# Performance work log

Measured on AMD Instinct MI355X. Metric: run time of the kernel, lower is better.

The kernel has to match this reference:

```python
import jax, jax.numpy as jnp
import numpy as np

D_MODEL = 1024
N_HEADS = 16
HEAD_DIM = D_MODEL // N_HEADS


def setup_inputs() -> dict:
    key = jax.random.key(0)
    k_x, k_qkv, k_out = jax.random.split(key, 3)
    x = jax.random.normal(k_x, (4, 2048, D_MODEL), dtype=jnp.float32)
    # nn.Linear weights are (out_features, in_features); init std=0.02
    w_qkv = jax.random.normal(k_qkv, (3 * D_MODEL, D_MODEL), dtype=jnp.float32) * 0.02
    w_out = jax.random.normal(k_out, (D_MODEL, D_MODEL), dtype=jnp.float32) * 0.02
    return {"x": x, "w_qkv": w_qkv, "w_out": w_out}


def reference(x, w_qkv, w_out):
    B, T, C = x.shape
    H, Dh = N_HEADS, HEAD_DIM
    # qkv projection: x @ w_qkv.T -> (B, T, 3C)
    qkv = jnp.einsum('btc,oc->bto', x, w_qkv)
    q, k, v = jnp.split(qkv, 3, axis=-1)

    def split_heads(t):
        return t.reshape(B, T, H, Dh).transpose(0, 2, 1, 3)  # (B, H, T, Dh)

    q, k, v = split_heads(q), split_heads(k), split_heads(v)
    scale = jnp.sqrt(jnp.asarray(Dh, dtype=x.dtype))
    scores = jnp.einsum('bhqd,bhkd->bhqk', q, k) / scale  # (B, H, T, T)
    causal = jnp.tril(jnp.ones((T, T), dtype=bool))
    scores = jnp.where(causal[None, None], scores, jnp.asarray(-jnp.inf, dtype=scores.dtype))
    attn = jax.nn.softmax(scores, axis=-1)
    out = jnp.einsum('bhqk,bhkd->bhqd', attn, v)  # (B, H, T, Dh)
    out = out.transpose(0, 2, 1, 3).reshape(B, T, C)
    return jnp.einsum('btc,oc->bto', out, w_out)
```

## Files before the change

### kernel.cpp

```cpp
#include <hip/hip_runtime.h>

typedef __attribute__((ext_vector_type(8))) short bf16x8;
typedef __attribute__((ext_vector_type(4))) float f32x4;
typedef __attribute__((ext_vector_type(16))) float f32x16;
typedef __attribute__((ext_vector_type(4))) int i32x4;
using u16 = unsigned short;

constexpr int Bsz = 4, T = 2048, C = 1024, H = 16, Dh = 64;
constexpr int Mrows = Bsz * T;
constexpr int K_DIM = 1024;
constexpr float QSCALE = 0.18033688011112042f;

__device__ inline u16 f2bf(float f) {
    unsigned u = __builtin_bit_cast(unsigned, f);
    u += 0x7FFFu + ((u >> 16) & 1u);
    return (u16)(u >> 16);
}

__device__ inline void g2l16(const void* g, void* l) {
    __builtin_amdgcn_global_load_lds((const __attribute__((address_space(1))) void*)g,
                                     (__attribute__((address_space(3))) void*)l, 16, 0, 0);
}

__device__ inline unsigned pk2(float lo, float hi) {
    unsigned d;
    asm("v_cvt_pk_bf16_f32 %0, %1, %2" : "=v"(d) : "v"(lo), "v"(hi));
    return d;
}
__device__ inline void swap32(unsigned& a, unsigned& b) {
    asm("v_permlane32_swap_b32 %0, %1" : "+v"(a), "+v"(b));
}

__global__ __launch_bounds__(256)
void cvt_k(const float* __restrict__ x, const float* __restrict__ wq,
           const float* __restrict__ wo, u16* __restrict__ xb,
           u16* __restrict__ wqb, u16* __restrict__ wob)
{
    int idx = blockIdx.x * 256 + threadIdx.x;
    const float* src; u16* dst; int rel;
    if (idx < 1048576)      { src = x;  dst = xb;  rel = idx; }
    else if (idx < 1441792) { src = wq; dst = wqb; rel = idx - 1048576; }
    else                    { src = wo; dst = wob; rel = idx - 1441792; }
    size_t off = (size_t)rel * 8;
    float4 a = *(const float4*)(src + off);
    float4 b = *(const float4*)(src + off + 4);
    unsigned r0 = (unsigned)f2bf(a.x) | ((unsigned)f2bf(a.y) << 16);
    unsigned r1 = (unsigned)f2bf(a.z) | ((unsigned)f2bf(a.w) << 16);
    unsigned r2 = (unsigned)f2bf(b.x) | ((unsigned)f2bf(b.y) << 16);
    unsigned r3 = (unsigned)f2bf(b.z) | ((unsigned)f2bf(b.w) << 16);
    *(uint4*)(dst + off) = make_uint4(r0, r1, r2, r3);
}

__device__ inline void stage_g(u16* lds, const u16* gb, int ldg, int tid) {
    #pragma unroll
    for (int i = 0; i < 4; ++i) {
        int ch = i * 256 + tid;
        int r = ch >> 3, c8 = ch & 7;
        int sc = c8 ^ (r & 7);
        g2l16(gb + (size_t)r * ldg + sc * 8, lds + (i * 256 + (tid & 192)) * 8);
    }
}

template<int MODE>
__device__ __forceinline__
void gemm_body(const u16* __restrict__ Ab, const u16* __restrict__ Bb,
               float* __restrict__ Op, u16* __restrict__ qws,
               u16* __restrict__ kws, u16* __restrict__ vtws,
               u16* As, u16* Bs, int m0, int n0)
{
    const int tid = threadIdx.x;
    const int l = tid & 63, wid = tid >> 6;
    const int wm = wid >> 1, wn = wid & 1;
    const int lane16 = l & 15, lhi = l >> 4;

    const u16* Abase = Ab + (size_t)m0 * K_DIM;
    const u16* Bbase = Bb + (size_t)n0 * K_DIM;

    f32x4 acc[4][4] = {};

    for (int ks = 0; ks < K_DIM / 64; ++ks) {
        __syncthreads();
        stage_g(As, Abase + ks * 64, K_DIM, tid);
        stage_g(Bs, Bbase + ks * 64, K_DIM, tid);
        __syncthreads();
        #pragma unroll
        for (int kc = 0; kc < 2; kc++) {
            bf16x8 af[4], bfr[4];
            #pragma unroll
            for (int mi = 0; mi < 4; mi++) {
                int row = wm * 64 + mi * 16 + lane16;
                int byte = row * 128 + kc * 64 + lhi * 16; byte ^= (row & 7) << 4;
                af[mi] = *(const bf16x8*)((const char*)As + byte);
            }
            #pragma unroll
            for (int ni = 0; ni < 4; ni++) {
                int row = wn * 64 + ni * 16 + lane16;
                int byte = row * 128 + kc * 64 + lhi * 16; byte ^= (row & 7) << 4;
                bfr[ni] = *(const bf16x8*)((const char*)Bs + byte);
            }
            #pragma unroll
            for (int mi = 0; mi < 4; mi++)
                #pragma unroll
                for (int ni = 0; ni < 4; ni++) {
                    if constexpr (MODE == 2)
                        acc[mi][ni] = __builtin_amdgcn_mfma_f32_16x16x32_bf16(
                            bfr[ni], af[mi], acc[mi][ni], 0, 0, 0);
                    else
                        acc[mi][ni] = __builtin_amdgcn_mfma_f32_16x16x32_bf16(
                            af[mi], bfr[ni], acc[mi][ni], 0, 0, 0);
                }
        }
    }

    if constexpr (MODE == 2) {
        #pragma unroll
        for (int mi = 0; mi < 4; mi++)
            #pragma unroll
            for (int ni = 0; ni < 4; ni++)
                #pragma unroll
                for (int r = 0; r < 4; r++) {
                    int wr = n0 + wn * 64 + ni * 16 + lhi * 4 + r;
                    int tg = m0 + wm * 64 + mi * 16 + lane16;
                    int hh = (wr >> 6) & 15, d = wr & 63;
                    int bb = tg >> 11, tt = tg & 2047;
                    size_t off = (((size_t)bb * H + hh) * Dh + d) * T + tt;
                    vtws[off] = f2bf(acc[mi][ni][r]);
                }
    } else {
        #pragma unroll
        for (int mi = 0; mi < 4; mi++)
            #pragma unroll
            for (int ni = 0; ni < 4; ni++)
                #pragma unroll
                for (int r = 0; r < 4; r++) {
                    int gm = m0 + wm * 64 + mi * 16 + lhi * 4 + r;
                    int gn = n0 + wn * 64 + ni * 16 + lane16;
                    float val = acc[mi][ni][r];
                    if constexpr (MODE == 0) {
                        int hh = (gn >> 6) & 15, d = gn & 63;
                        int bb = gm >> 11, t = gm & 2047;
                        size_t off = (((size_t)bb * H + hh) * T + t) * Dh + d;
                        if (gn < C) qws[off] = f2bf(val * QSCALE);
                        else        kws[off] = f2bf(val);
                    } else {
                        Op[(size_t)gm * C + gn] = val;
                    }
                }
    }
}

__global__ __launch_bounds__(256)
void gemm_qkv(const u16* __restrict__ xb, const u16* __restrict__ wqkvb,
              u16* __restrict__ qws, u16* __restrict__ kws, u16* __restrict__ vtws)
{
    __shared__ alignas(16) u16 As[128 * 64];
    __shared__ alignas(16) u16 Bs[128 * 64];
    const int m0 = blockIdx.x * 128;
    if (blockIdx.y < 16)
        gemm_body<0>(xb, wqkvb, nullptr, qws, kws, vtws, As, Bs, m0, blockIdx.y * 128);
    else
        gemm_body<2>(xb, wqkvb, nullptr, qws, kws, vtws, As, Bs, m0,
                     2 * C + (blockIdx.y - 16) * 128);
}

__global__ __launch_bounds__(256)
void gemm_out(const u16* __restrict__ ob, const u16* __restrict__ woutb,
              float* __restrict__ Op)
{
    __shared__ alignas(16) u16 As[128 * 64];
    __shared__ alignas(16) u16 Bs[128 * 64];
    gemm_body<1>(ob, woutb, Op, nullptr, nullptr, nullptr, As, Bs,
                 blockIdx.x * 128, blockIdx.y * 128);
}

constexpr float SMAX = 16.0f;

__device__ inline void stage_c(u16* lds, const u16* gb, int rstride, int tid) {
    #pragma unroll
    for (int it = 0; it < 2; ++it) {
        int i = it * 256 + tid;
        int r = i & 63, c8 = i >> 6;
        g2l16(gb + (size_t)r * rstride + c8 * 8, lds + i * 8);
    }
}

__global__ __launch_bounds__(256, 3)
void attn_k(const u16* __restrict__ qws, const u16* __restrict__ kws,
            const u16* __restrict__ vtws, u16* __restrict__ ows)
{
    __shared__ alignas(16) u16 KL[3][64 * 64];
    __shared__ alignas(16) u16 VL[3][64 * 64];

    const int bid = blockIdx.x;
    const int head = bid & 63;
    const int qt = 15 - (bid >> 6);
    const int b = head >> 4, h = head & 15;
    const int tid = threadIdx.x, w = tid >> 6, l = tid & 63;
    const int l31 = l & 31, hi = l >> 5;

    const size_t hoff = (size_t)head * (T * Dh);
    const u16* Qg  = qws + hoff;
    const u16* Kg  = kws + hoff;
    const u16* Vtg = vtws + hoff;

    const int qb = qt * 128;
    const int nt = 2 * qt + 2;
    const int qbw = qb + w * 32;

    bf16x8 qf[4];
    #pragma unroll
    for (int c = 0; c < 4; ++c)
        qf[c] = *(const bf16x8*)(Qg + (size_t)(qbw + l31) * Dh + c * 16 + hi * 8);

    f32x16 o0{}, o1{};
    float lrun = 0.f;

    stage_c(KL[0], Kg, Dh, tid);
    stage_c(VL[0], Vtg, T, tid);
    stage_c(KL[1], Kg + (size_t)64 * Dh, Dh, tid);
    stage_c(VL[1], Vtg + 64, T, tid);

    int cur = 0;
    for (int t = 0; t < nt; ++t) {
        if (t + 1 < nt) asm volatile("s_waitcnt vmcnt(4)" ::: "memory");
        else            asm volatile("s_waitcnt vmcnt(0)" ::: "memory");
        __builtin_amdgcn_s_barrier();
        __builtin_amdgcn_sched_barrier(0);

        int nx = cur + 2; if (nx >= 3) nx -= 3;
        if (t + 2 < nt) {
            stage_c(KL[nx], Kg + (size_t)(t + 2) * 64 * Dh, Dh, tid);
            stage_c(VL[nx], Vtg + (t + 2) * 64, T, tid);
        }

        const int kv0 = t * 64;
        if (kv0 <= qbw + 31) {
            const char* Kb = (const char*)KL[cur];
            const char* Vb = (const char*)VL[cur];

            bf16x8 kf0[4], kf1[4];
            #pragma unroll
            for (int c = 0; c < 4; ++c) {
                int off = (c * 2 + hi) * 1024 + l31 * 16;
                kf0[c] = *(const bf16x8*)(Kb + off);
                kf1[c] = *(const bf16x8*)(Kb + off + 512);
            }

            f32x16 s0{}, s1{};
            __builtin_amdgcn_s_setprio(1);
            #pragma unroll
            for (int c = 0; c < 4; ++c) {
                s0 = __builtin_amdgcn_mfma_f32_32x32x16_bf16(kf0[c], qf[c], s0, 0, 0, 0);
                s1 = __builtin_amdgcn_mfma_f32_32x32x16_bf16(kf1[c], qf[c], s1, 0, 0, 0);
            }
            __builtin_amdgcn_s_setprio(0);

            if (kv0 + 63 > qbw) {
                int qg = qbw + l31;
                #pragma unroll
                for (int r = 0; r < 16; ++r) {
                    int kvg = kv0 + (r & 3) + 8 * (r >> 2) + 4 * hi;
                    if (kvg > qg)      s0[r] = -__builtin_inff();
                    if (kvg + 32 > qg) s1[r] = -__builtin_inff();
                }
            }

            float p0[16], p1[16];
            float t0 = 0.f, t1 = 0.f, t2 = 0.f, t3 = 0.f;
            #pragma unroll
            for (int r = 0; r < 16; ++r) {
                p0[r] = __builtin_amdgcn_exp2f(s0[r] - SMAX);
                p1[r] = __builtin_amdgcn_exp2f(s1[r] - SMAX);
                float s = p0[r] + p1[r];
                if ((r & 3) == 0) t0 += s; else if ((r & 3) == 1) t1 += s;
                else if ((r & 3) == 2) t2 += s; else t3 += s;
            }
            lrun += (t0 + t1) + (t2 + t3);

            unsigned paf[4][4];
            unsigned cc[8];
            #pragma unroll
            for (int i = 0; i < 4; ++i) cc[i]     = pk2(p0[2 * i], p0[2 * i + 1]);
            #pragma unroll
            for (int i = 0; i < 4; ++i) cc[4 + i] = pk2(p0[8 + 2 * i], p0[9 + 2 * i]);
            swap32(cc[0], cc[2]); swap32(cc[1], cc[3]);
            swap32(cc[4], cc[6]); swap32(cc[5], cc[7]);
            #pragma unroll
            for (int i = 0; i < 4; ++i) { paf[0][i] = cc[i]; paf[1][i] = cc[4 + i]; }
            #pragma unroll
            for (int i = 0; i < 4; ++i) cc[i]     = pk2(p1[2 * i], p1[2 * i + 1]);
            #pragma unroll
            for (int i = 0; i < 4; ++i) cc[4 + i] = pk2(p1[8 + 2 * i], p1[9 + 2 * i]);
            swap32(cc[0], cc[2]); swap32(cc[1], cc[3]);
            swap32(cc[4], cc[6]); swap32(cc[5], cc[7]);
            #pragma unroll
            for (int i = 0; i < 4; ++i) { paf[2][i] = cc[i]; paf[3][i] = cc[4 + i]; }

            __builtin_amdgcn_s_setprio(1);
            #pragma unroll
            for (int kb = 0; kb < 4; ++kb) {
                i32x4 wv = {(int)paf[kb][0], (int)paf[kb][1],
                            (int)paf[kb][2], (int)paf[kb][3]};
                bf16x8 pa = __builtin_bit_cast(bf16x8, wv);
                int off = (kb * 2 + hi) * 1024 + l31 * 16;
                bf16x8 v0 = *(const bf16x8*)(Vb + off);
                bf16x8 v1 = *(const bf16x8*)(Vb + off + 512);
                o0 = __builtin_amdgcn_mfma_f32_32x32x16_bf16(pa, v0, o0, 0, 0, 0);
                o1 = __builtin_amdgcn_mfma_f32_32x32x16_bf16(pa, v1, o1, 0, 0, 0);
            }
            __builtin_amdgcn_s_setprio(0);
        }
        cur = (cur == 2) ? 0 : cur + 1;
    }

    float lt = lrun + __shfl_xor(lrun, 32);
    float inv = 1.0f / lt;
    #pragma unroll
    for (int r = 0; r < 16; ++r) {
        int cr = (r & 3) + 8 * (r >> 2) + 4 * hi;
        float il = __shfl(inv, cr);
        size_t rowoff = ((size_t)b * T + qb + w * 32 + cr) * C + h * Dh + l31;
        ows[rowoff]      = f2bf(o0[r] * il);
        ows[rowoff + 32] = f2bf(o1[r] * il);
    }
}

extern "C" void kernel_launch(void* const* d_in, const int* in_sizes, int n_in,
                              void* d_out, int out_size, void* d_ws, size_t ws_size,
                              hipStream_t stream)
{
    const float* x     = (const float*)d_in[0];
    const float* w_qkv = (const float*)d_in[1];
    const float* w_out = (const float*)d_in[2];
    float* out = (float*)d_out;

    const size_t SZ = (size_t)Bsz * H * T * Dh;
    u16* qws   = (u16*)d_ws;
    u16* kws   = qws + SZ;
    u16* vtws  = kws + SZ;
    u16* xb    = vtws + SZ;
    u16* ows   = xb;
    u16* wqkvb = xb + SZ;
    u16* woutb = wqkvb + (size_t)3 * C * C;

    cvt_k<<<dim3(6144), 256, 0, stream>>>(x, w_qkv, w_out, xb, wqkvb, woutb);

    gemm_qkv<<<dim3(Mrows / 128, 24), 256, 0, stream>>>(xb, wqkvb, qws, kws, vtws);

    attn_k<<<dim3(1024), 256, 0, stream>>>(qws, kws, vtws, ows);

    gemm_out<<<dim3(Mrows / 128, C / 128), 256, 0, stream>>>(ows, woutb, out);
}
```

Baseline: 157.2 us.

## Split QKV GEMM into pipelined 256x256 QK kernel and separate V kernel

Moves the Q and K projections into a new 512-thread kernel with 256x256 tiles and double-buffered LDS. It interleaves async global-to-LDS loads with MFMA phases, using explicit barriers, vmcnt waits and setprio to overlap memory and compute. The V projection, with its transposed store, stays on the old 128x128 path as its own launch. This is meant to raise MFMA utilisation and data reuse for the larger part of the QKV GEMM. The cost is an extra kernel launch, much higher register pressure from 128 accumulators per thread, and fragile hand-written synchronisation.

Measured after the change: 154.9 us, median of 4. No clear change (-1.4%).

```diff
diff --git a/kernel.cpp b/kernel.cpp
--- a/kernel.cpp
+++ b/kernel.cpp
@@ -51,6 +51,182 @@
     *(uint4*)(dst + off) = make_uint4(r0, r1, r2, r3);
 }
 
+__device__ __forceinline__ bf16x8 rdfrag(const u16* base, int row, int kc, int lhi) {
+    int byte = row * 128 + kc * 64 + lhi * 16;
+    byte ^= (row & 7) << 4;
+    return *(const bf16x8*)((const char*)base + byte);
+}
+
+__device__ __forceinline__ void stg_half(u16* ldsbase, const u16* gb, int tid) {
+    #pragma unroll
+    for (int it2 = 0; it2 < 2; ++it2) {
+        int i = it2 * 512 + tid;
+        int r = i >> 3, c8 = i & 7;
+        int sc = c8 ^ (r & 7);
+        g2l16(gb + (size_t)r * K_DIM + sc * 8,
+              ldsbase + (size_t)(it2 * 512 + (tid & 448)) * 8);
+    }
+}
+
+__device__ __forceinline__ void rdAf(bf16x8 (&af)[4][2], const u16* base,
+                                     int r0, int lane16, int lhi) {
+    #pragma unroll
+    for (int mi = 0; mi < 4; ++mi)
+        #pragma unroll
+        for (int kc = 0; kc < 2; ++kc)
+            af[mi][kc] = rdfrag(base, r0 + mi * 16 + lane16, kc, lhi);
+}
+
+__device__ __forceinline__ void rdBf(bf16x8 (&bf2)[2][2], const u16* base,
+                                     int r0, int lane16, int lhi) {
+    #pragma unroll
+    for (int ni = 0; ni < 2; ++ni)
+        #pragma unroll
+        for (int kc = 0; kc < 2; ++kc)
+            bf2[ni][kc] = rdfrag(base, r0 + ni * 16 + lane16, kc, lhi);
+}
+
+__device__ __forceinline__ void mfma_quad(f32x4 (&acc)[8][4], const bf16x8 (&af)[4][2],
+                                          const bf16x8 (&bf2)[2][2], int rh, int ch) {
+    #pragma unroll
+    for (int kc = 0; kc < 2; ++kc)
+        #pragma unroll
+        for (int mi = 0; mi < 4; ++mi)
+            #pragma unroll
+            for (int ni = 0; ni < 2; ++ni)
+                acc[rh * 4 + mi][ch * 2 + ni] = __builtin_amdgcn_mfma_f32_16x16x32_bf16(
+                    af[mi][kc], bf2[ni][kc], acc[rh * 4 + mi][ch * 2 + ni], 0, 0, 0);
+}
+
+__device__ __forceinline__ void ph_open() {
+    __builtin_amdgcn_s_barrier();
+    asm volatile("s_waitcnt lgkmcnt(0)" ::: "memory");
+    __builtin_amdgcn_sched_barrier(0);
+}
+__device__ __forceinline__ void ph_close() {
+    __builtin_amdgcn_s_barrier();
+    __builtin_amdgcn_sched_barrier(0);
+}
+
+__global__ __launch_bounds__(512, 2)
+void gemm_qk8(const u16* __restrict__ xb, const u16* __restrict__ wqkvb,
+              u16* __restrict__ qws, u16* __restrict__ kws)
+{
+    __shared__ alignas(16) u16 As[2][256 * 64];
+    __shared__ alignas(16) u16 Bs2[2][256 * 64];
+
+    const int tid = threadIdx.x;
+    const int l = tid & 63, wid = tid >> 6;
+    const int wm = wid >> 2, wn = wid & 3;
+    const int lane16 = l & 15, lhi = l >> 4;
+    const int m0 = blockIdx.x * 256, n0 = blockIdx.y * 256;
+
+    const u16* Ab = xb + (size_t)m0 * K_DIM;
+    const u16* Bb = wqkvb + (size_t)n0 * K_DIM;
+
+    f32x4 acc[8][4] = {};
+    bf16x8 af[4][2];
+    bf16x8 bfr[2][2][2];
+
+    stg_half(&As[0][0],     Ab, tid);
+    stg_half(&As[0][8192],  Ab + (size_t)128 * K_DIM, tid);
+    stg_half(&Bs2[0][0],    Bb, tid);
+    stg_half(&Bs2[0][8192], Bb + (size_t)128 * K_DIM, tid);
+    stg_half(&Bs2[1][0],    Bb + 64, tid);
+    asm volatile("s_waitcnt vmcnt(2)" ::: "memory");
+    __builtin_amdgcn_s_barrier();
+    __builtin_amdgcn_sched_barrier(0);
+
+    for (int it = 0; it < 8; ++it) {
+        const int ka = it * 128;
+        const bool more = (it < 7);
+
+        rdAf(af, As[0], wm * 128, lane16, lhi);
+        rdBf(bfr[0], Bs2[0], wn * 64, lane16, lhi);
+        stg_half(&Bs2[1][8192], Bb + (size_t)128 * K_DIM + ka + 64, tid);
+        ph_open();
+        __builtin_amdgcn_s_setprio(1);
+        mfma_quad(acc, af, bfr[0], 0, 0);
+        __builtin_amdgcn_s_setprio(0);
+        ph_close();
+
+        rdBf(bfr[1], Bs2[0], wn * 64 + 32, lane16, lhi);
+        stg_half(&As[1][0], Ab + ka + 64, tid);
+        ph_open();
+        __builtin_amdgcn_s_setprio(1);
+        mfma_quad(acc, af, bfr[1], 0, 1);
+        __builtin_amdgcn_s_setprio(0);
+        ph_close();
+
+        rdAf(af, As[0], wm * 128 + 64, lane16, lhi);
+        stg_half(&As[1][8192], Ab + (size_t)128 * K_DIM + ka + 64, tid);
+        ph_open();
+        __builtin_amdgcn_s_setprio(1);
+        mfma_quad(acc, af, bfr[1], 1, 1);
+        __builtin_amdgcn_s_setprio(0);
+        ph_close();
+
+        if (more) stg_half(&Bs2[0][0], Bb + ka + 128, tid);
+        ph_open();
+        __builtin_amdgcn_s_setprio(1);
+        mfma_quad(acc, af, bfr[0], 1, 0);
+        __builtin_amdgcn_s_setprio(0);
+        if (more) asm volatile("s_waitcnt vmcnt(2)" ::: "memory");
+        else      asm volatile("s_waitcnt vmcnt(0)" ::: "memory");
+        ph_close();
+
+        rdAf(af, As[1], wm * 128, lane16, lhi);
+        rdBf(bfr[0], Bs2[1], wn * 64, lane16, lhi);
+        if (more) stg_half(&Bs2[0][8192], Bb + (size_t)128 * K_DIM + ka + 128, tid);
+        ph_open();
+        __builtin_amdgcn_s_setprio(1);
+        mfma_quad(acc, af, bfr[0], 0, 0);
+        __builtin_amdgcn_s_setprio(0);
+        ph_close();
+
+        rdBf(bfr[1], Bs2[1], wn * 64 + 32, lane16, lhi);
+        if (more) stg_half(&As[0][0], Ab + ka + 128, tid);
+        ph_open();
+        __builtin_amdgcn_s_setprio(1);
+        mfma_quad(acc, af, bfr[1], 0, 1);
+        __builtin_amdgcn_s_setprio(0);
+        ph_close();
+
+        rdAf(af, As[1], wm * 128 + 64, lane16, lhi);
+        if (more) stg_half(&As[0][8192], Ab + (size_t)128 * K_DIM + ka + 128, tid);
+        ph_open();
+        __builtin_amdgcn_s_setprio(1);
+        mfma_quad(acc, af, bfr[1], 1, 1);
+        __builtin_amdgcn_s_setprio(0);
+        ph_close();
+
+        if (more) stg_half(&Bs2[1][0], Bb + ka + 192, tid);
+        ph_open();
+        __builtin_amdgcn_s_setprio(1);
+        mfma_quad(acc, af, bfr[0], 1, 0);
+        __builtin_amdgcn_s_setprio(0);
+        if (more) asm volatile("s_waitcnt vmcnt(2)" ::: "memory");
+        else      asm volatile("s_waitcnt vmcnt(0)" ::: "memory");
+        ph_close();
+    }
+
+    #pragma unroll
+    for (int a = 0; a < 8; ++a)
+        #pragma unroll
+        for (int bc = 0; bc < 4; ++bc)
+            #pragma unroll
+            for (int r = 0; r < 4; ++r) {
+                int gm = m0 + wm * 128 + a * 16 + lhi * 4 + r;
+                int gn = n0 + wn * 64 + bc * 16 + lane16;
+                float val = acc[a][bc][r];
+                int hh = (gn >> 6) & 15, d = gn & 63;
+                int bb = gm >> 11, t = gm & 2047;
+                size_t off = (((size_t)bb * H + hh) * T + t) * Dh + d;
+                if (gn < C) qws[off] = f2bf(val * QSCALE);
+                else        kws[off] = f2bf(val);
+            }
+}
+
 __device__ inline void stage_g(u16* lds, const u16* gb, int ldg, int tid) {
     #pragma unroll
     for (int i = 0; i < 4; ++i) {
@@ -64,8 +240,7 @@
 template<int MODE>
 __device__ __forceinline__
 void gemm_body(const u16* __restrict__ Ab, const u16* __restrict__ Bb,
-               float* __restrict__ Op, u16* __restrict__ qws,
-               u16* __restrict__ kws, u16* __restrict__ vtws,
+               float* __restrict__ Op, u16* __restrict__ vtws,
                u16* As, u16* Bs, int m0, int n0)
 {
     const int tid = threadIdx.x;
@@ -135,32 +310,19 @@
                 for (int r = 0; r < 4; r++) {
                     int gm = m0 + wm * 64 + mi * 16 + lhi * 4 + r;
                     int gn = n0 + wn * 64 + ni * 16 + lane16;
-                    float val = acc[mi][ni][r];
-                    if constexpr (MODE == 0) {
-                        int hh = (gn >> 6) & 15, d = gn & 63;
-                        int bb = gm >> 11, t = gm & 2047;
-                        size_t off = (((size_t)bb * H + hh) * T + t) * Dh + d;
-                        if (gn < C) qws[off] = f2bf(val * QSCALE);
-                        else        kws[off] = f2bf(val);
-                    } else {
-                        Op[(size_t)gm * C + gn] = val;
-                    }
+                    Op[(size_t)gm * C + gn] = acc[mi][ni][r];
                 }
     }
 }
 
 __global__ __launch_bounds__(256)
-void gemm_qkv(const u16* __restrict__ xb, const u16* __restrict__ wqkvb,
-              u16* __restrict__ qws, u16* __restrict__ kws, u16* __restrict__ vtws)
+void gemm_v(const u16* __restrict__ xb, const u16* __restrict__ wqkvb,
+            u16* __restrict__ vtws)
 {
     __shared__ alignas(16) u16 As[128 * 64];
     __shared__ alignas(16) u16 Bs[128 * 64];
-    const int m0 = blockIdx.x * 128;
-    if (blockIdx.y < 16)
-        gemm_body<0>(xb, wqkvb, nullptr, qws, kws, vtws, As, Bs, m0, blockIdx.y * 128);
-    else
-        gemm_body<2>(xb, wqkvb, nullptr, qws, kws, vtws, As, Bs, m0,
-                     2 * C + (blockIdx.y - 16) * 128);
+    gemm_body<2>(xb, wqkvb, nullptr, vtws, As, Bs,
+                 blockIdx.x * 128, 2 * C + blockIdx.y * 128);
 }
 
 __global__ __launch_bounds__(256)
@@ -169,7 +331,7 @@
 {
     __shared__ alignas(16) u16 As[128 * 64];
     __shared__ alignas(16) u16 Bs[128 * 64];
-    gemm_body<1>(ob, woutb, Op, nullptr, nullptr, nullptr, As, Bs,
+    gemm_body<1>(ob, woutb, Op, nullptr, As, Bs,
                  blockIdx.x * 128, blockIdx.y * 128);
 }
 
@@ -345,7 +507,8 @@
 
     cvt_k<<<dim3(6144), 256, 0, stream>>>(x, w_qkv, w_out, xb, wqkvb, woutb);
 
-    gemm_qkv<<<dim3(Mrows / 128, 24), 256, 0, stream>>>(xb, wqkvb, qws, kws, vtws);
+    gemm_qk8<<<dim3(Mrows / 256, (2 * C) / 256), 512, 0, stream>>>(xb, wqkvb, qws, kws);
+    gemm_v<<<dim3(Mrows / 128, C / 128), 256, 0, stream>>>(xb, wqkvb, vtws);
 
     attn_k<<<dim3(1024), 256, 0, stream>>>(qws, kws, vtws, ows);
 
```
